# Kernel optimization log

Hardware: AMD Instinct MI355X
Metric: run time of the kernel (lower is better)

## Reference

```python
import jax, jax.numpy as jnp
import numpy as np

B, NQ, NK, DM, H, DK = 8, 1024, 1024, 512, 8, 64


def setup_inputs() -> dict:
    key = jax.random.key(0)
    ks = jax.random.split(key, 20)
    s = 1.0 / np.sqrt(DM)
    inp = {
        "queries": jax.random.normal(ks[0], (B, NQ, DM), jnp.float32),
        "keys": jax.random.normal(ks[1], (B, NK, DM), jnp.float32),
        "values": jax.random.normal(ks[2], (B, NK, DM), jnp.float32),
        "attention_mask": jax.random.randint(ks[3], (B, H, NQ, NK), 0, 2).astype(bool),
        "attention_weights": jax.random.uniform(ks[4], (B, H, NQ, NK), jnp.float32),
        "memory": jax.random.uniform(ks[5], (B, NK), jnp.float32),
        "geometry": jax.random.uniform(ks[6], (B, H, NQ, NK), jnp.float32),
        "Wq": jax.random.normal(ks[7], (DM, H * DK), jnp.float32) * s,
        "bq": jnp.zeros((H * DK,), jnp.float32),
        "Wk": jax.random.normal(ks[8], (DM, H * DK), jnp.float32) * s,
        "bk": jnp.zeros((H * DK,), jnp.float32),
        "Wv": jax.random.normal(ks[9], (DM, H * DK), jnp.float32) * s,
        "bv": jnp.zeros((H * DK,), jnp.float32),
        "Wmm": jax.random.normal(ks[10], (1, H * DK), jnp.float32),
        "bmm": jnp.zeros((H * DK,), jnp.float32),
        "Wo": jax.random.normal(ks[11], (H * DK, DM), jnp.float32) * s,
        "bo": jnp.zeros((DM,), jnp.float32),
    }
    return inp


def reference(queries, keys, values, attention_mask, attention_weights, memory,
              geometry, Wq, bq, Wk, bk, Wv, bv, Wmm, bmm, Wo, bo):
    b, nq = queries.shape[:2]
    nk = keys.shape[1]
    # projections -> (b, h, n, d)
    q = (queries @ Wq + bq).reshape(b, nq, H, DK).transpose(0, 2, 1, 3)
    k = (keys @ Wk + bk).reshape(b, nk, H, DK).transpose(0, 2, 1, 3)
    v = (values @ Wv + bv).reshape(b, nk, H, DK).transpose(0, 2, 1, 3)
    # memory gate: (b, nk, 1) @ (1, h*dk) -> (b, h, nk, dk)
    mm = (memory[..., None] @ Wmm + bmm).reshape(b, nk, H, DK).transpose(0, 2, 1, 3)
    # gated scores (b, h, nq, nk)
    att = jnp.einsum('bhqd,bhkd->bhqk', q, k * mm) / np.sqrt(DK)
    att = att * attention_weights
    att = jnp.where(attention_mask, -jnp.inf, att)
    # geometric log-bias + softmax
    w_mn = jax.nn.softmax(jnp.log(jnp.clip(geometry, 1e-6)) + att, axis=-1)
    out = jnp.einsum('bhqk,bhkd->bhqd', w_mn, v * mm)
    out = out.transpose(0, 2, 1, 3).reshape(b, nq, H * DK)
    return out @ Wo + bo
```

## Files before the change

kernel.cpp:

```cpp
#include <hip/hip_runtime.h>
#include <hip/hip_bf16.h>
#include <math.h>

#define B_ 8
#define NQ_ 1024
#define NK_ 1024
#define H_ 8
#define DK_ 64
#define HDK_ 512
#define LOG2E 1.4426950408889634f

typedef _Float16 half8 __attribute__((ext_vector_type(8)));
typedef _Float16 half4 __attribute__((ext_vector_type(4)));
typedef float f32x4 __attribute__((ext_vector_type(4)));

__global__ void detect_mask_kernel(const unsigned int* __restrict__ w, int nwords,
                                   int* __restrict__ flag) {
  __shared__ int s;
  if (threadIdx.x == 0) s = 0;
  __syncthreads();
  int bad = 0;
  for (int i = threadIdx.x; i < nwords; i += blockDim.x) {
    unsigned int v = w[i];
    if (v > 1u && v != 0x3F800000u) bad = 1;
  }
  if (bad) atomicOr(&s, 1);
  __syncthreads();
  if (threadIdx.x == 0) *flag = s;
}

__global__ __launch_bounds__(256)
void wtrans_kernel(const float* __restrict__ w0, const float* __restrict__ w1,
                   const float* __restrict__ w2, const float* __restrict__ w3,
                   _Float16* __restrict__ t0, _Float16* __restrict__ t1,
                   _Float16* __restrict__ t2, _Float16* __restrict__ t3) {
  __shared__ float tile[64][65];
  const float* W;
  _Float16* T;
  switch (blockIdx.y) {
    case 0: W = w0; T = t0; break;
    case 1: W = w1; T = t1; break;
    case 2: W = w2; T = t2; break;
    default: W = w3; T = t3; break;
  }
  const int t = blockIdx.x;
  const int k0 = (t >> 3) * 64, n0 = (t & 7) * 64;
  const int tid = threadIdx.x;
  const int r = tid >> 4, c4 = (tid & 15) * 4;
#pragma unroll
  for (int i = 0; i < 4; ++i) {
    const int kk = r + i * 16;
    float4 v = *(const float4*)(W + (size_t)(k0 + kk) * 512 + n0 + c4);
    tile[kk][c4 + 0] = v.x;
    tile[kk][c4 + 1] = v.y;
    tile[kk][c4 + 2] = v.z;
    tile[kk][c4 + 3] = v.w;
  }
  __syncthreads();
#pragma unroll
  for (int i = 0; i < 4; ++i) {
    const int nn = r + i * 16;
    half4 h;
#pragma unroll
    for (int j = 0; j < 4; ++j) h[j] = (_Float16)tile[c4 + j][nn];
    *(half4*)(T + (size_t)(n0 + nn) * 512 + k0 + c4) = h;
  }
}

__global__ __launch_bounds__(256)
void gemm_kernel(const float* __restrict__ A32, const _Float16* __restrict__ A16,
                 const _Float16* __restrict__ Bt, const float* __restrict__ bias,
                 const float* __restrict__ mem, const float* __restrict__ Wmm,
                 const float* __restrict__ bmm, void* __restrict__ outp,
                 const int mode) {
  __shared__ _Float16 As[128 * 32];
  __shared__ _Float16 Bs[128 * 32];
  const int tid = threadIdx.x;
  const int lane = tid & 63, wave = tid >> 6;
  const int wr = wave >> 1, wc = wave & 1;
  const int l15 = lane & 15, l4 = lane >> 4;
  const int row0 = blockIdx.x * 128, col0 = blockIdx.y * 128;
  const int srow = tid >> 1;
  const int sc0 = (tid & 1) * 2;

  f32x4 acc[4][4] = {};

  for (int k0 = 0; k0 < 512; k0 += 32) {
    __syncthreads();
    const _Float16* sb = Bt + (size_t)(col0 + srow) * 512 + k0;
#pragma unroll
    for (int c = 0; c < 2; ++c) {
      int ci = sc0 + c;
      half8 ha;
      if (mode == 3) {
        ha = *(const half8*)(A16 + (size_t)(row0 + srow) * 512 + k0 + ci * 8);
      } else {
        const float* s = A32 + (size_t)(row0 + srow) * 512 + k0 + ci * 8;
        float4 x = *(const float4*)s;
        float4 y = *(const float4*)(s + 4);
        ha[0] = (_Float16)x.x; ha[1] = (_Float16)x.y;
        ha[2] = (_Float16)x.z; ha[3] = (_Float16)x.w;
        ha[4] = (_Float16)y.x; ha[5] = (_Float16)y.y;
        ha[6] = (_Float16)y.z; ha[7] = (_Float16)y.w;
      }
      float4 vb = *(const float4*)(sb + ci * 8);
      int cd = ci ^ (srow & 3);
      *(half8*)((char*)As + srow * 64 + (cd << 4)) = ha;
      *(float4*)((char*)Bs + srow * 64 + (cd << 4)) = vb;
    }
    __syncthreads();
    half8 af[4], bf[4];
#pragma unroll
    for (int mi = 0; mi < 4; ++mi) {
      int r = wr * 64 + mi * 16 + l15;
      af[mi] = *(half8*)((char*)As + r * 64 + ((l4 ^ (r & 3)) << 4));
    }
#pragma unroll
    for (int ni = 0; ni < 4; ++ni) {
      int r = wc * 64 + ni * 16 + l15;
      bf[ni] = *(half8*)((char*)Bs + r * 64 + ((l4 ^ (r & 3)) << 4));
    }
#pragma unroll
    for (int mi = 0; mi < 4; ++mi)
#pragma unroll
      for (int ni = 0; ni < 4; ++ni)
        acc[mi][ni] =
            __builtin_amdgcn_mfma_f32_16x16x32_f16(af[mi], bf[ni], acc[mi][ni], 0, 0, 0);
  }

#pragma unroll
  for (int mi = 0; mi < 4; ++mi) {
#pragma unroll
    for (int ni = 0; ni < 4; ++ni) {
      const int gc = col0 + wc * 64 + ni * 16 + l15;
      const float bi = bias[gc];
      const int h = gc >> 6, d = gc & 63;
#pragma unroll
      for (int reg = 0; reg < 4; ++reg) {
        const int gr = row0 + wr * 64 + mi * 16 + l4 * 4 + reg;
        float val = acc[mi][ni][reg] + bi;
        if (mode == 3) {
          ((float*)outp)[(size_t)gr * 512 + gc] = val;
        } else if (mode == 0) {
          const int b = gr >> 10, n = gr & 1023;
          ((_Float16*)outp)[((size_t)(b * 8 + h) * 1024 + n) * 64 + d] =
              (_Float16)(val * (LOG2E / 8.0f));
        } else {
          const int b = gr >> 10, n = gr & 1023;
          float mmv = fmaf(mem[gr], Wmm[gc], bmm[gc]);
          float g = val * mmv;
          if (mode == 1)
            ((_Float16*)outp)[((size_t)(b * 8 + h) * 1024 + n) * 64 + d] = (_Float16)g;
          else
            ((_Float16*)outp)[((size_t)(b * 8 + h) * 64 + d) * 1024 + n] = (_Float16)g;
        }
      }
    }
  }
}

__global__ __launch_bounds__(256, 2)
void attn_kernel(const _Float16* __restrict__ Qp, const _Float16* __restrict__ Kg,
                 const _Float16* __restrict__ Vgt, const float* __restrict__ attw,
                 const float* __restrict__ geom, const void* __restrict__ maskp,
                 const int* __restrict__ flagp, _Float16* __restrict__ Ocat) {
  __shared__ _Float16 Kbuf[2][64 * 64];
  __shared__ _Float16 Ps[4][16 * 64];

  const int tid = threadIdx.x;
  const int lane = tid & 63, wave = tid >> 6;
  const int l15 = lane & 15, l4 = lane >> 4;
  const int bid = blockIdx.x;
  const int qt = bid >> 6;
  const int g = bid & 63;
  const int h = g & 7, b = g >> 3;
  const int bh = b * H_ + h;
  const int qb = qt * 64 + wave * 16;
  const int kq = qb + l15;
  const int maskBytes = *flagp;
  const unsigned char* m8 = (const unsigned char*)maskp;
  const int* m32 = (const int*)maskp;

  half8 aq[2];
  {
    const _Float16* qsrc = Qp + ((size_t)bh * NQ_ + kq) * DK_;
#pragma unroll
    for (int s = 0; s < 2; ++s) aq[s] = *(const half8*)(qsrc + s * 32 + l4 * 8);
  }

  f32x4 fo[4] = {};
  float mrun = -INFINITY, lrun = 0.f;

  const size_t wgBase = ((size_t)bh << 20) + (size_t)kq * NK_ + l4 * 4;
  const _Float16* Vbase = Vgt + (size_t)bh * DK_ * NK_;

  const int srL = lane >> 3;
  const int sci = lane & 7;
  auto stageK = [&](int kt, int sel) {
    const char* kgb = (const char*)(Kg + ((size_t)bh * NK_ + kt * 64) * DK_);
#pragma unroll
    for (int i = 0; i < 2; ++i) {
      const int rbase = wave * 16 + i * 8;
      const int r = rbase + srL;
      const char* src = kgb + (size_t)r * 128 + ((sci ^ (r & 7)) << 4);
      __builtin_amdgcn_global_load_lds(src, (char*)&Kbuf[sel][0] + rbase * 128, 16, 0, 0);
    }
  };

  half8 vfrag[2][4];
  auto loadV = [&](int kt) {
#pragma unroll
    for (int s4 = 0; s4 < 2; ++s4)
#pragma unroll
      for (int c = 0; c < 4; ++c)
        vfrag[s4][c] = *(const half8*)(Vbase + (size_t)(c * 16 + l15) * NK_ +
                                       kt * 64 + s4 * 32 + l4 * 8);
  };

  float4 wv[4], gv[4];
  unsigned mk;
  auto loadWG = [&](int kt) {
    const size_t base = wgBase + (size_t)kt * 64;
    unsigned m = 0;
#pragma unroll
    for (int c = 0; c < 4; ++c) {
      wv[c] = *(const float4*)(attw + base + c * 16);
      gv[c] = *(const float4*)(geom + base + c * 16);
      if (maskBytes) {
        unsigned v = *(const unsigned*)(m8 + base + c * 16);
        m |= (((v & 0xffu) ? 1u : 0u) | ((v & 0xff00u) ? 2u : 0u) |
              ((v & 0xff0000u) ? 4u : 0u) | ((v & 0xff000000u) ? 8u : 0u)) << (c * 4);
      } else {
        int4 v = *(const int4*)(m32 + base + c * 16);
        m |= ((v.x ? 1u : 0u) | (v.y ? 2u : 0u) | (v.z ? 4u : 0u) | (v.w ? 8u : 0u))
             << (c * 4);
      }
    }
    mk = m;
  };

  stageK(0, 0);
  loadWG(0);
  __syncthreads();

#pragma unroll 2
  for (int kt = 0; kt < 16; ++kt) {
    const int sel = kt & 1;
    if (kt + 1 < 16) stageK(kt + 1, sel ^ 1);
    loadV(kt);

    const char* Kb = (const char*)&Kbuf[sel][0];

    f32x4 sf[4];
    __builtin_amdgcn_s_setprio(1);
#pragma unroll
    for (int c = 0; c < 4; ++c) {
      sf[c] = (f32x4){0.f, 0.f, 0.f, 0.f};
#pragma unroll
      for (int s = 0; s < 2; ++s) {
        int r = c * 16 + l15;
        half8 ak = *(half8*)(Kb + r * 128 + (((s * 4 + l4) ^ (r & 7)) << 4));
        sf[c] = __builtin_amdgcn_mfma_f32_16x16x32_f16(ak, aq[s], sf[c], 0, 0, 0);
      }
    }
    __builtin_amdgcn_s_setprio(0);

#pragma unroll
    for (int c = 0; c < 4; ++c) {
#pragma unroll
      for (int reg = 0; reg < 4; ++reg) {
        float t;
        if ((mk >> (c * 4 + reg)) & 1u)
          t = -INFINITY;
        else
          t = fmaf(sf[c][reg], wv[c][reg], __log2f(fmaxf(gv[c][reg], 1e-6f)));
        sf[c][reg] = t;
      }
    }

    if (kt + 1 < 16) loadWG(kt + 1);

    float mx = -INFINITY;
#pragma unroll
    for (int c = 0; c < 4; ++c)
#pragma unroll
      for (int reg = 0; reg < 4; ++reg) mx = fmaxf(mx, sf[c][reg]);
    mx = fmaxf(mx, __shfl_xor(mx, 16));
    mx = fmaxf(mx, __shfl_xor(mx, 32));
    const float mn = fmaxf(mrun, mx);
    const float sc = (mrun == -INFINITY) ? 0.f : exp2f(mrun - mn);
    mrun = mn;

    float rs = 0.f;
#pragma unroll
    for (int c = 0; c < 4; ++c)
#pragma unroll
      for (int reg = 0; reg < 4; ++reg) {
        float t = sf[c][reg];
        float p = (t == -INFINITY) ? 0.f : exp2f(t - mn);
        sf[c][reg] = p;
        rs += p;
      }
#pragma unroll
    for (int c = 0; c < 4; ++c)
#pragma unroll
      for (int reg = 0; reg < 4; ++reg) fo[c][reg] *= sc;
    lrun = lrun * sc + rs;

    char* pw = (char*)&Ps[wave][0];
#pragma unroll
    for (int c = 0; c < 4; ++c) {
      half4 hp;
#pragma unroll
      for (int reg = 0; reg < 4; ++reg) hp[reg] = (_Float16)sf[c][reg];
      int ci = c * 2 + (l4 >> 1);
      *(half4*)(pw + l15 * 128 + ((ci ^ (l15 & 7)) << 4) + (l4 & 1) * 8) = hp;
    }

    __builtin_amdgcn_s_setprio(1);
#pragma unroll
    for (int s4 = 0; s4 < 2; ++s4) {
      half8 bp = *(half8*)(pw + l15 * 128 + (((s4 * 4 + l4) ^ (l15 & 7)) << 4));
#pragma unroll
      for (int c = 0; c < 4; ++c)
        fo[c] = __builtin_amdgcn_mfma_f32_16x16x32_f16(vfrag[s4][c], bp, fo[c], 0, 0, 0);
    }
    __builtin_amdgcn_s_setprio(0);

    __syncthreads();
  }

  float lsum = lrun;
  lsum += __shfl_xor(lsum, 16);
  lsum += __shfl_xor(lsum, 32);
  const float rinv = 1.0f / lsum;

  _Float16* orow = Ocat + ((size_t)b * NQ_ + qb + l15) * HDK_ + h * DK_;
#pragma unroll
  for (int c = 0; c < 4; ++c) {
    half4 hv;
#pragma unroll
    for (int reg = 0; reg < 4; ++reg) hv[reg] = (_Float16)(fo[c][reg] * rinv);
    *(half4*)(orow + c * 16 + l4 * 4) = hv;
  }
}

extern "C" void kernel_launch(void* const* d_in, const int* in_sizes, int n_in,
                              void* d_out, int out_size, void* d_ws, size_t ws_size,
                              hipStream_t stream) {
  (void)in_sizes; (void)n_in; (void)out_size; (void)ws_size;
  const float* queries = (const float*)d_in[0];
  const float* keys    = (const float*)d_in[1];
  const float* values  = (const float*)d_in[2];
  const void*  maskp   = d_in[3];
  const float* attw    = (const float*)d_in[4];
  const float* memo    = (const float*)d_in[5];
  const float* geom    = (const float*)d_in[6];
  const float* Wq = (const float*)d_in[7];
  const float* bq = (const float*)d_in[8];
  const float* Wk = (const float*)d_in[9];
  const float* bk = (const float*)d_in[10];
  const float* Wv = (const float*)d_in[11];
  const float* bv = (const float*)d_in[12];
  const float* Wmm = (const float*)d_in[13];
  const float* bmm = (const float*)d_in[14];
  const float* Wo = (const float*)d_in[15];
  const float* bo = (const float*)d_in[16];

  char* ws = (char*)d_ws;
  size_t off = 0;
  auto alloc = [&](size_t bytes) {
    char* p = ws + off;
    off += (bytes + 255) & ~(size_t)255;
    return p;
  };
  const size_t MAT = (size_t)8192 * 512 * 2;
  int* flag = (int*)alloc(256);
  _Float16* Wtq = (_Float16*)alloc((size_t)512 * 512 * 2);
  _Float16* Wtk = (_Float16*)alloc((size_t)512 * 512 * 2);
  _Float16* Wtv = (_Float16*)alloc((size_t)512 * 512 * 2);
  _Float16* Wto = (_Float16*)alloc((size_t)512 * 512 * 2);
  _Float16* Qp   = (_Float16*)alloc(MAT);
  _Float16* Kgp  = (_Float16*)alloc(MAT);
  _Float16* Vgtp = (_Float16*)alloc(MAT);
  _Float16* Ocat = (_Float16*)alloc(MAT);

  detect_mask_kernel<<<1, 256, 0, stream>>>((const unsigned int*)maskp, 4096, flag);
  wtrans_kernel<<<dim3(64, 4), 256, 0, stream>>>(Wq, Wk, Wv, Wo, Wtq, Wtk, Wtv, Wto);

  dim3 ggrid(64, 4);
  gemm_kernel<<<ggrid, 256, 0, stream>>>(queries, nullptr, Wtq, bq, nullptr, nullptr,
                                         nullptr, Qp, 0);
  gemm_kernel<<<ggrid, 256, 0, stream>>>(keys, nullptr, Wtk, bk, memo, Wmm, bmm, Kgp, 1);
  gemm_kernel<<<ggrid, 256, 0, stream>>>(values, nullptr, Wtv, bv, memo, Wmm, bmm,
                                         Vgtp, 2);

  attn_kernel<<<1024, 256, 0, stream>>>(Qp, Kgp, Vgtp, attw, geom, maskp, flag, Ocat);

  gemm_kernel<<<ggrid, 256, 0, stream>>>(nullptr, Ocat, Wto, bo, nullptr, nullptr,
                                         nullptr, d_out, 3);
}
```

Baseline: 386.9 us.

## Batch QKV GEMMs, fold mask detect, stage V via LDS, use geometry multiplicatively

Merges the mask-detection kernel into the weight-transpose launch and runs the Q/K/V projection GEMMs as a single launch using blockIdx.z, which cuts launch count. In the attention kernel, V tiles are now double-buffered into LDS with async global-to-LDS loads alongside K, replacing direct per-lane global loads. The per-element log2 of geometry is replaced by multiplying the exponentiated score by the clamped geometry, which removes a transcendental per element. Masking is applied after the exponent instead of before. The running max no longer includes the geometry bias, so range and rounding behaviour change slightly, and LDS use grows, which may lower occupancy.

```diff
diff --git a/kernel.cpp b/kernel.cpp
--- a/kernel.cpp
+++ b/kernel.cpp
@@ -14,27 +14,29 @@
 typedef _Float16 half4 __attribute__((ext_vector_type(4)));
 typedef float f32x4 __attribute__((ext_vector_type(4)));
 
-__global__ void detect_mask_kernel(const unsigned int* __restrict__ w, int nwords,
-                                   int* __restrict__ flag) {
-  __shared__ int s;
-  if (threadIdx.x == 0) s = 0;
-  __syncthreads();
-  int bad = 0;
-  for (int i = threadIdx.x; i < nwords; i += blockDim.x) {
-    unsigned int v = w[i];
-    if (v > 1u && v != 0x3F800000u) bad = 1;
-  }
-  if (bad) atomicOr(&s, 1);
-  __syncthreads();
-  if (threadIdx.x == 0) *flag = s;
-}
-
 __global__ __launch_bounds__(256)
 void wtrans_kernel(const float* __restrict__ w0, const float* __restrict__ w1,
                    const float* __restrict__ w2, const float* __restrict__ w3,
                    _Float16* __restrict__ t0, _Float16* __restrict__ t1,
-                   _Float16* __restrict__ t2, _Float16* __restrict__ t3) {
+                   _Float16* __restrict__ t2, _Float16* __restrict__ t3,
+                   const unsigned int* __restrict__ maskw, int nwords,
+                   int* __restrict__ flag) {
   __shared__ float tile[64][65];
+  if (blockIdx.x == 64) {
+    if (blockIdx.y != 0) return;
+    __shared__ int s;
+    if (threadIdx.x == 0) s = 0;
+    __syncthreads();
+    int bad = 0;
+    for (int i = threadIdx.x; i < nwords; i += blockDim.x) {
+      unsigned int v = maskw[i];
+      if (v > 1u && v != 0x3F800000u) bad = 1;
+    }
+    if (bad) atomicOr(&s, 1);
+    __syncthreads();
+    if (threadIdx.x == 0) *flag = s;
+    return;
+  }
   const float* W;
   _Float16* T;
   switch (blockIdx.y) {
@@ -68,13 +70,23 @@
 }
 
 __global__ __launch_bounds__(256)
-void gemm_kernel(const float* __restrict__ A32, const _Float16* __restrict__ A16,
-                 const _Float16* __restrict__ Bt, const float* __restrict__ bias,
+void gemm_kernel(const float* __restrict__ A0, const float* __restrict__ A1,
+                 const float* __restrict__ A2, const _Float16* __restrict__ A16,
+                 const _Float16* __restrict__ B0, const _Float16* __restrict__ B1,
+                 const _Float16* __restrict__ B2, const float* __restrict__ bias0,
+                 const float* __restrict__ bias1, const float* __restrict__ bias2,
                  const float* __restrict__ mem, const float* __restrict__ Wmm,
-                 const float* __restrict__ bmm, void* __restrict__ outp,
-                 const int mode) {
+                 const float* __restrict__ bmm, void* __restrict__ out0,
+                 void* __restrict__ out1, void* __restrict__ out2,
+                 const int mode_base) {
   __shared__ _Float16 As[128 * 32];
   __shared__ _Float16 Bs[128 * 32];
+  const int mode = mode_base + blockIdx.z;
+  const float* A32 = (mode == 1) ? A1 : (mode == 2) ? A2 : A0;
+  const _Float16* Bt = (mode == 1) ? B1 : (mode == 2) ? B2 : B0;
+  const float* bias = (mode == 1) ? bias1 : (mode == 2) ? bias2 : bias0;
+  void* outp = (mode == 1) ? out1 : (mode == 2) ? out2 : out0;
+
   const int tid = threadIdx.x;
   const int lane = tid & 63, wave = tid >> 6;
   const int wr = wave >> 1, wc = wave & 1;
@@ -165,6 +177,7 @@
                  const float* __restrict__ geom, const void* __restrict__ maskp,
                  const int* __restrict__ flagp, _Float16* __restrict__ Ocat) {
   __shared__ _Float16 Kbuf[2][64 * 64];
+  __shared__ _Float16 Vbuf[2][64 * 64];
   __shared__ _Float16 Ps[4][16 * 64];
 
   const int tid = threadIdx.x;
@@ -192,12 +205,12 @@
   float mrun = -INFINITY, lrun = 0.f;
 
   const size_t wgBase = ((size_t)bh << 20) + (size_t)kq * NK_ + l4 * 4;
-  const _Float16* Vbase = Vgt + (size_t)bh * DK_ * NK_;
 
   const int srL = lane >> 3;
   const int sci = lane & 7;
-  auto stageK = [&](int kt, int sel) {
+  auto stageKV = [&](int kt, int sel) {
     const char* kgb = (const char*)(Kg + ((size_t)bh * NK_ + kt * 64) * DK_);
+    const char* vgb = (const char*)(Vgt + (size_t)bh * DK_ * NK_ + kt * 64);
 #pragma unroll
     for (int i = 0; i < 2; ++i) {
       const int rbase = wave * 16 + i * 8;
@@ -205,16 +218,13 @@
       const char* src = kgb + (size_t)r * 128 + ((sci ^ (r & 7)) << 4);
       __builtin_amdgcn_global_load_lds(src, (char*)&Kbuf[sel][0] + rbase * 128, 16, 0, 0);
     }
-  };
-
-  half8 vfrag[2][4];
-  auto loadV = [&](int kt) {
-#pragma unroll
-    for (int s4 = 0; s4 < 2; ++s4)
-#pragma unroll
-      for (int c = 0; c < 4; ++c)
-        vfrag[s4][c] = *(const half8*)(Vbase + (size_t)(c * 16 + l15) * NK_ +
-                                       kt * 64 + s4 * 32 + l4 * 8);
+#pragma unroll
+    for (int i = 0; i < 2; ++i) {
+      const int rbase = wave * 16 + i * 8;
+      const int r = rbase + srL;
+      const char* src = vgb + (size_t)r * (NK_ * 2) + ((sci ^ (r & 7)) << 4);
+      __builtin_amdgcn_global_load_lds(src, (char*)&Vbuf[sel][0] + rbase * 128, 16, 0, 0);
+    }
   };
 
   float4 wv[4], gv[4];
@@ -239,17 +249,17 @@
     mk = m;
   };
 
-  stageK(0, 0);
+  stageKV(0, 0);
   loadWG(0);
   __syncthreads();
 
 #pragma unroll 2
   for (int kt = 0; kt < 16; ++kt) {
     const int sel = kt & 1;
-    if (kt + 1 < 16) stageK(kt + 1, sel ^ 1);
-    loadV(kt);
+    if (kt + 1 < 16) stageKV(kt + 1, sel ^ 1);
 
     const char* Kb = (const char*)&Kbuf[sel][0];
+    const char* Vb = (const char*)&Vbuf[sel][0];
 
     f32x4 sf[4];
     __builtin_amdgcn_s_setprio(1);
@@ -265,26 +275,15 @@
     }
     __builtin_amdgcn_s_setprio(0);
 
-#pragma unroll
-    for (int c = 0; c < 4; ++c) {
+    float mx = -INFINITY;
+#pragma unroll
+    for (int c = 0; c < 4; ++c)
 #pragma unroll
       for (int reg = 0; reg < 4; ++reg) {
-        float t;
-        if ((mk >> (c * 4 + reg)) & 1u)
-          t = -INFINITY;
-        else
-          t = fmaf(sf[c][reg], wv[c][reg], __log2f(fmaxf(gv[c][reg], 1e-6f)));
-        sf[c][reg] = t;
-      }
-    }
-
-    if (kt + 1 < 16) loadWG(kt + 1);
-
-    float mx = -INFINITY;
-#pragma unroll
-    for (int c = 0; c < 4; ++c)
-#pragma unroll
-      for (int reg = 0; reg < 4; ++reg) mx = fmaxf(mx, sf[c][reg]);
+        float sv = sf[c][reg] * wv[c][reg];
+        sf[c][reg] = sv;
+        mx = fmaxf(mx, sv);
+      }
     mx = fmaxf(mx, __shfl_xor(mx, 16));
     mx = fmaxf(mx, __shfl_xor(mx, 32));
     const float mn = fmaxf(mrun, mx);
@@ -296,11 +295,14 @@
     for (int c = 0; c < 4; ++c)
 #pragma unroll
       for (int reg = 0; reg < 4; ++reg) {
-        float t = sf[c][reg];
-        float p = (t == -INFINITY) ? 0.f : exp2f(t - mn);
+        float p = fmaxf(gv[c][reg], 1e-6f) * exp2f(sf[c][reg] - mn);
+        p = ((mk >> (c * 4 + reg)) & 1u) ? 0.f : p;
         sf[c][reg] = p;
         rs += p;
       }
+
+    if (kt + 1 < 16) loadWG(kt + 1);
+
 #pragma unroll
     for (int c = 0; c < 4; ++c)
 #pragma unroll
@@ -320,10 +322,13 @@
     __builtin_amdgcn_s_setprio(1);
 #pragma unroll
     for (int s4 = 0; s4 < 2; ++s4) {
-      half8 bp = *(half8*)(pw + l15 * 128 + (((s4 * 4 + l4) ^ (l15 & 7)) << 4));
-#pragma unroll
-      for (int c = 0; c < 4; ++c)
-        fo[c] = __builtin_amdgcn_mfma_f32_16x16x32_f16(vfrag[s4][c], bp, fo[c], 0, 0, 0);
+      half8 pa = *(half8*)(pw + l15 * 128 + (((s4 * 4 + l4) ^ (l15 & 7)) << 4));
+#pragma unroll
+      for (int c = 0; c < 4; ++c) {
+        int rd = c * 16 + l15;
+        half8 bv = *(half8*)(Vb + rd * 128 + (((s4 * 4 + l4) ^ (rd & 7)) << 4));
+        fo[c] = __builtin_amdgcn_mfma_f32_16x16x32_f16(bv, pa, fo[c], 0, 0, 0);
+      }
     }
     __builtin_amdgcn_s_setprio(0);
 
@@ -335,7 +340,7 @@
   lsum += __shfl_xor(lsum, 32);
   const float rinv = 1.0f / lsum;
 
-  _Float16* orow = Ocat + ((size_t)b * NQ_ + qb + l15) * HDK_ + h * DK_;
+  _Float16* orow = Ocat + ((size_t)b * NQ_ + kq) * HDK_ + h * DK_;
 #pragma unroll
   for (int c = 0; c < 4; ++c) {
     half4 hv;
@@ -385,18 +390,16 @@
   _Float16* Vgtp = (_Float16*)alloc(MAT);
   _Float16* Ocat = (_Float16*)alloc(MAT);
 
-  detect_mask_kernel<<<1, 256, 0, stream>>>((const unsigned int*)maskp, 4096, flag);
-  wtrans_kernel<<<dim3(64, 4), 256, 0, stream>>>(Wq, Wk, Wv, Wo, Wtq, Wtk, Wtv, Wto);
-
-  dim3 ggrid(64, 4);
-  gemm_kernel<<<ggrid, 256, 0, stream>>>(queries, nullptr, Wtq, bq, nullptr, nullptr,
-                                         nullptr, Qp, 0);
-  gemm_kernel<<<ggrid, 256, 0, stream>>>(keys, nullptr, Wtk, bk, memo, Wmm, bmm, Kgp, 1);
-  gemm_kernel<<<ggrid, 256, 0, stream>>>(values, nullptr, Wtv, bv, memo, Wmm, bmm,
-                                         Vgtp, 2);
+  wtrans_kernel<<<dim3(65, 4), 256, 0, stream>>>(Wq, Wk, Wv, Wo, Wtq, Wtk, Wtv, Wto,
+                                                 (const unsigned int*)maskp, 4096, flag);
+
+  gemm_kernel<<<dim3(64, 4, 3), 256, 0, stream>>>(
+      queries, keys, values, nullptr, Wtq, Wtk, Wtv, bq, bk, bv, memo, Wmm, bmm,
+      Qp, Kgp, Vgtp, 0);
 
   attn_kernel<<<1024, 256, 0, stream>>>(Qp, Kgp, Vgtp, attw, geom, maskp, flag, Ocat);
 
-  gemm_kernel<<<ggrid, 256, 0, stream>>>(nullptr, Ocat, Wto, bo, nullptr, nullptr,
-                                         nullptr, d_out, 3);
+  gemm_kernel<<<dim3(64, 4, 1), 256, 0, stream>>>(
+      nullptr, nullptr, nullptr, Ocat, Wto, nullptr, nullptr, bo, nullptr, nullptr,
+      nullptr, nullptr, nullptr, d_out, nullptr, nullptr, 3);
 }
```

Result: faster. 319.9 us (median of 2 runs) (-17.3%).
